# Optimization experiments

Hardware: AMD Instinct MI355X
Metric: run time of the kernel (lower is better)

The kernel has to match this reference:

```python
import jax, jax.numpy as jnp
import numpy as np

B, T, C, H = 512, 256, 512, 64  # batch, block_size, n_embedding, head_size


def setup_inputs() -> dict:
    key = jax.random.key(0)
    kx, kq, kk, kv = jax.random.split(key, 4)
    # nn.Linear(C, H, bias=False) default init ~ U(-1/sqrt(C), 1/sqrt(C)); stored as x @ W
    s = 1.0 / np.sqrt(C)
    return {
        "x": jax.random.normal(kx, (B, T, C), dtype=jnp.float32),
        "Wq": jax.random.uniform(kq, (C, H), jnp.float32, -s, s),
        "Wk": jax.random.uniform(kk, (C, H), jnp.float32, -s, s),
        "Wv": jax.random.uniform(kv, (C, H), jnp.float32, -s, s),
    }


def reference(x, Wq, Wk, Wv):
    # Projections (bias=False Linear)
    q = x @ Wq  # [B,T,H]
    k = x @ Wk  # [B,T,H]
    v = x @ Wv  # [B,T,H]
    scale = k.shape[-1] ** -0.5
    wei = jnp.einsum('bqh,bkh->bqk', q, k) * scale  # [B,T,T]
    causal = jnp.tril(jnp.ones((x.shape[1], x.shape[1]), dtype=bool))
    wei = jnp.where(causal, wei, -jnp.inf)
    wei = jax.nn.softmax(wei, axis=-1)
    # dropout p=0.0 (eval-mode reference) -> identity
    return wei @ v  # [B,T,H]
```

## Files before the change

### kernel.cpp

```cpp
#include <hip/hip_runtime.h>
#include <hip/hip_bf16.h>

typedef __bf16 bf16;
typedef __bf16 bf16x8 __attribute__((ext_vector_type(8)));
typedef __bf16 bf16x4 __attribute__((ext_vector_type(4)));
typedef float  f32x4  __attribute__((ext_vector_type(4)));

#define MFMA16(a,b,c) __builtin_amdgcn_mfma_f32_16x16x32_bf16((a),(b),(c),0,0,0)

__device__ __forceinline__ void gld16(const void* g, void* l) {
    __builtin_amdgcn_global_load_lds(
        (const __attribute__((address_space(1))) void*)g,
        (__attribute__((address_space(3))) void*)l, 16, 0, 0);
}


__global__ void __launch_bounds__(256) wt_frag_kernel(
        const float* __restrict__ Wq, const float* __restrict__ Wk,
        const float* __restrict__ Wv, bf16* __restrict__ WTfrag) {
    int tid = blockIdx.x * 256 + threadIdx.x;
    int j  = tid & 7;
    int l  = (tid >> 3) & 63;
    int f  = tid >> 9;
    int nf = f % 12;
    int KC = f / 12;
    int k   = KC * 32 + (l >> 4) * 8 + j;
    int col = (nf & 3) * 16 + (l & 15);
    const float* W = (nf < 4) ? Wq : ((nf < 8) ? Wk : Wv);
    WTfrag[tid] = (bf16)W[k * 64 + col];
}

__global__ void __launch_bounds__(256, 2) fused_kernel(
        const float* __restrict__ x, const bf16* __restrict__ WTfrag,
        float* __restrict__ out) {
    extern __shared__ char smem[];

    const int tid = threadIdx.x;
    const int l   = tid & 63;
    const int w   = tid >> 6;
    const int lo  = l & 15;
    const int hi  = l >> 4;
    const int b   = blockIdx.x;
    const char* xb = (const char*)x + (size_t)b * 524288;
    const char* wb = (const char*)WTfrag;

    f32x4 acc[4][12];
    #pragma unroll
    for (int mq = 0; mq < 4; ++mq)
        #pragma unroll
        for (int nf = 0; nf < 12; ++nf)
            acc[mq][nf] = (f32x4){0.f, 0.f, 0.f, 0.f};

    #pragma unroll 1
    for (int kc = 0; kc < 16; ++kc) {
        #pragma unroll
        for (int j = 0; j < 8; ++j) {
            const int s   = j * 256 + tid;
            const int row = s >> 3;
            const int uP  = s & 7;
            const int uL  = uP ^ (row & 7);
            gld16(xb + (size_t)row * 2048 + kc * 128 + uL * 16,
                  smem + s * 16);
        }
        #pragma unroll
        for (int j = 0; j < 3; ++j) {
            const int s = j * 256 + tid;
            gld16(wb + kc * 12288 + s * 16, smem + 32768 + s * 16);
        }
        __syncthreads();

        bf16x8 a[4];
        #pragma unroll
        for (int mq = 0; mq < 4; ++mq) {
            const int row = mq * 64 + w * 16 + lo;
            const int u0  = (hi * 2)     ^ (lo & 7);
            const int u1  = (hi * 2 + 1) ^ (lo & 7);
            f32x4 v0 = *(const f32x4*)(smem + row * 128 + u0 * 16);
            f32x4 v1 = *(const f32x4*)(smem + row * 128 + u1 * 16);
            bf16x8 t;
            t[0] = (bf16)v0[0]; t[1] = (bf16)v0[1]; t[2] = (bf16)v0[2]; t[3] = (bf16)v0[3];
            t[4] = (bf16)v1[0]; t[5] = (bf16)v1[1]; t[6] = (bf16)v1[2]; t[7] = (bf16)v1[3];
            a[mq] = t;
        }
        #pragma unroll
        for (int nf = 0; nf < 12; ++nf) {
            bf16x8 bf_ = *(const bf16x8*)(smem + 32768 + nf * 1024 + l * 16);
            #pragma unroll
            for (int mq = 0; mq < 4; ++mq)
                acc[mq][nf] = MFMA16(a[mq], bf_, acc[mq][nf]);
        }
        __syncthreads();
    }

    char* Kb = smem;
    char* Vb = smem + 32768;
    #pragma unroll
    for (int nf = 4; nf < 12; ++nf) {
        #pragma unroll
        for (int mq = 0; mq < 4; ++mq) {
            #pragma unroll
            for (int i = 0; i < 4; ++i) {
                bf16 v = (bf16)acc[mq][nf][i];
                if (nf < 8) {
                    const int row = mq * 64 + w * 16 + hi * 4 + i;
                    const int col = (nf - 4) * 16 + lo;
                    const int u   = col >> 3;
                    *(bf16*)(Kb + row * 128 + ((u ^ (row & 7)) << 4) +
                             (col & 7) * 2) = v;
                } else {
                    const int h = (nf - 8) * 16 + lo;
                    const int t = mq * 64 + w * 16 + hi * 4 + i;
                    const int u = t >> 3;
                    *(bf16*)(Vb + h * 512 + ((u ^ (h & 7)) << 4) +
                             (t & 7) * 2) = v;
                }
            }
        }
    }

    bf16* Pl = (bf16*)(smem + 65536) + w * 1152;
    bf16x8 qfr[4][2];
    #pragma unroll
    for (int qf = 0; qf < 4; ++qf) {
        #pragma unroll
        for (int nf = 0; nf < 4; ++nf)
            #pragma unroll
            for (int i = 0; i < 4; ++i)
                Pl[(hi * 4 + i) * 72 + nf * 16 + lo] = (bf16)acc[qf][nf][i];
        __syncthreads();
        #pragma unroll
        for (int ks = 0; ks < 2; ++ks)
            qfr[qf][ks] = *(const bf16x8*)(Pl + lo * 72 + ks * 32 + hi * 8);
        __syncthreads();
    }

    f32x4 o[4][4];
    #pragma unroll
    for (int qf = 0; qf < 4; ++qf)
        #pragma unroll
        for (int mf = 0; mf < 4; ++mf)
            o[qf][mf] = (f32x4){0.f, 0.f, 0.f, 0.f};
    float m2[4]   = {-INFINITY, -INFINITY, -INFINITY, -INFINITY};
    float lsum[4] = {0.f, 0.f, 0.f, 0.f};

    const float SC = 0.125f * 1.44269504088896340736f;

    #pragma unroll
    for (int kc = 0; kc < 4; ++kc) {
        bf16x8 vf[4][2];
        #pragma unroll
        for (int mf = 0; mf < 4; ++mf)
            #pragma unroll
            for (int ks = 0; ks < 2; ++ks) {
                const int h = mf * 16 + lo;
                const int u = kc * 8 + ks * 4 + hi;
                vf[mf][ks] = *(const bf16x8*)(Vb + h * 512 + ((u ^ (lo & 7)) << 4));
            }

        #pragma unroll
        for (int qf = kc; qf < 4; ++qf) {
            f32x4 s[4];
            #pragma unroll
            for (int kf = 0; kf < 4; ++kf) {
                const int key = kc * 64 + kf * 16 + lo;
                bf16x8 k0 = *(const bf16x8*)(Kb + key * 128 + ((hi ^ (lo & 7)) << 4));
                bf16x8 k1 = *(const bf16x8*)(Kb + key * 128 + (((4 + hi) ^ (lo & 7)) << 4));
                f32x4 t = (f32x4){0.f, 0.f, 0.f, 0.f};
                t = MFMA16(k0, qfr[qf][0], t);
                t = MFMA16(k1, qfr[qf][1], t);
                s[kf] = t;
            }
            float mx = -INFINITY;
            #pragma unroll
            for (int kf = 0; kf < 4; ++kf)
                #pragma unroll
                for (int i = 0; i < 4; ++i) {
                    float v = s[kf][i] * SC;
                    if (kc == qf && (kf * 16 + hi * 4 + i) > (w * 16 + lo)) v = -INFINITY;
                    s[kf][i] = v;
                    mx = fmaxf(mx, v);
                }
            mx = fmaxf(mx, __shfl_xor(mx, 16));
            mx = fmaxf(mx, __shfl_xor(mx, 32));
            const float mnew = fmaxf(m2[qf], mx);
            const float rsc  = exp2f(m2[qf] - mnew);
            m2[qf] = mnew;

            float cs = 0.f;
            bf16x4 pk[4];
            #pragma unroll
            for (int kf = 0; kf < 4; ++kf)
                #pragma unroll
                for (int i = 0; i < 4; ++i) {
                    float p = exp2f(s[kf][i] - mnew);
                    cs += p;
                    pk[kf][i] = (bf16)p;
                }
            cs += __shfl_xor(cs, 16);
            cs += __shfl_xor(cs, 32);
            lsum[qf] = lsum[qf] * rsc + cs;

            #pragma unroll
            for (int kf = 0; kf < 4; ++kf)
                *(bf16x4*)(Pl + lo * 72 + kf * 16 + hi * 4) = pk[kf];

            #pragma unroll
            for (int mf = 0; mf < 4; ++mf) {
                o[qf][mf][0] *= rsc; o[qf][mf][1] *= rsc;
                o[qf][mf][2] *= rsc; o[qf][mf][3] *= rsc;
            }
            #pragma unroll
            for (int ks = 0; ks < 2; ++ks) {
                bf16x8 pf = *(const bf16x8*)(Pl + lo * 72 + ks * 32 + hi * 8);
                #pragma unroll
                for (int mf = 0; mf < 4; ++mf)
                    o[qf][mf] = MFMA16(vf[mf][ks], pf, o[qf][mf]);
            }
        }
    }

    #pragma unroll
    for (int qf = 0; qf < 4; ++qf) {
        const float inv = 1.0f / lsum[qf];
        const int q = qf * 64 + w * 16 + lo;
        #pragma unroll
        for (int mf = 0; mf < 4; ++mf) {
            f32x4 r4;
            r4[0] = o[qf][mf][0] * inv; r4[1] = o[qf][mf][1] * inv;
            r4[2] = o[qf][mf][2] * inv; r4[3] = o[qf][mf][3] * inv;
            *(f32x4*)(out + (b * 256 + q) * 64 + mf * 16 + hi * 4) = r4;
        }
    }
}

extern "C" void kernel_launch(void* const* d_in, const int* in_sizes, int n_in,
                              void* d_out, int out_size, void* d_ws, size_t ws_size,
                              hipStream_t stream) {
    const float* x  = (const float*)d_in[0];
    const float* Wq = (const float*)d_in[1];
    const float* Wk = (const float*)d_in[2];
    const float* Wv = (const float*)d_in[3];
    float* out = (float*)d_out;

    bf16* WTfrag = (bf16*)d_ws;

    wt_frag_kernel<<<dim3(384), dim3(256), 0, stream>>>(Wq, Wk, Wv, WTfrag);
    fused_kernel<<<dim3(512), dim3(256), 74752, stream>>>(x, WTfrag, out);
}
```

Measured before the change: 71.81 us.

## Double-buffer x tiles in LDS and load weight fragments directly to registers

The projection loop now prefetches the next x chunk into a second LDS buffer while the current chunk is used for MFMA, so global load latency can overlap compute. Weight fragments are read straight from global memory into registers instead of being staged through LDS. The intent is to cut the exposed load latency and one barrier per iteration. The cost is higher register pressure (12 B fragments held live) and per-wave global reads of the weights, which are repeated across waves.

```diff
diff --git a/kernel.cpp b/kernel.cpp
--- a/kernel.cpp
+++ b/kernel.cpp
@@ -51,43 +51,47 @@
         for (int nf = 0; nf < 12; ++nf)
             acc[mq][nf] = (f32x4){0.f, 0.f, 0.f, 0.f};
 
+    #pragma unroll
+    for (int j = 0; j < 8; ++j) {
+        const int s   = j * 256 + tid;
+        const int row = s >> 3;
+        const int uL  = (s & 7) ^ (row & 7);
+        gld16(xb + (size_t)row * 2048 + 0 * 128 + uL * 16, smem + s * 16);
+    }
+    __syncthreads();
+
     #pragma unroll 1
     for (int kc = 0; kc < 16; ++kc) {
-        #pragma unroll
-        for (int j = 0; j < 8; ++j) {
-            const int s   = j * 256 + tid;
-            const int row = s >> 3;
-            const int uP  = s & 7;
-            const int uL  = uP ^ (row & 7);
-            gld16(xb + (size_t)row * 2048 + kc * 128 + uL * 16,
-                  smem + s * 16);
-        }
-        #pragma unroll
-        for (int j = 0; j < 3; ++j) {
-            const int s = j * 256 + tid;
-            gld16(wb + kc * 12288 + s * 16, smem + 32768 + s * 16);
-        }
-        __syncthreads();
-
-        bf16x8 a[4];
+        bf16x8 bfr[12];
+        #pragma unroll
+        for (int nf = 0; nf < 12; ++nf)
+            bfr[nf] = *(const bf16x8*)(wb + (kc * 12 + nf) * 1024 + l * 16);
+        __builtin_amdgcn_sched_barrier(0);
+        if (kc < 15) {
+            #pragma unroll
+            for (int j = 0; j < 8; ++j) {
+                const int s   = j * 256 + tid;
+                const int row = s >> 3;
+                const int uL  = (s & 7) ^ (row & 7);
+                gld16(xb + (size_t)row * 2048 + (kc + 1) * 128 + uL * 16,
+                      smem + ((kc + 1) & 1) * 32768 + s * 16);
+            }
+        }
+        __builtin_amdgcn_sched_barrier(0);
+        const char* xlds = smem + (kc & 1) * 32768;
         #pragma unroll
         for (int mq = 0; mq < 4; ++mq) {
             const int row = mq * 64 + w * 16 + lo;
             const int u0  = (hi * 2)     ^ (lo & 7);
             const int u1  = (hi * 2 + 1) ^ (lo & 7);
-            f32x4 v0 = *(const f32x4*)(smem + row * 128 + u0 * 16);
-            f32x4 v1 = *(const f32x4*)(smem + row * 128 + u1 * 16);
-            bf16x8 t;
-            t[0] = (bf16)v0[0]; t[1] = (bf16)v0[1]; t[2] = (bf16)v0[2]; t[3] = (bf16)v0[3];
-            t[4] = (bf16)v1[0]; t[5] = (bf16)v1[1]; t[6] = (bf16)v1[2]; t[7] = (bf16)v1[3];
-            a[mq] = t;
-        }
-        #pragma unroll
-        for (int nf = 0; nf < 12; ++nf) {
-            bf16x8 bf_ = *(const bf16x8*)(smem + 32768 + nf * 1024 + l * 16);
-            #pragma unroll
-            for (int mq = 0; mq < 4; ++mq)
-                acc[mq][nf] = MFMA16(a[mq], bf_, acc[mq][nf]);
+            f32x4 v0 = *(const f32x4*)(xlds + row * 128 + u0 * 16);
+            f32x4 v1 = *(const f32x4*)(xlds + row * 128 + u1 * 16);
+            bf16x8 a;
+            a[0] = (bf16)v0[0]; a[1] = (bf16)v0[1]; a[2] = (bf16)v0[2]; a[3] = (bf16)v0[3];
+            a[4] = (bf16)v1[0]; a[5] = (bf16)v1[1]; a[6] = (bf16)v1[2]; a[7] = (bf16)v1[3];
+            #pragma unroll
+            for (int nf = 0; nf < 12; ++nf)
+                acc[mq][nf] = MFMA16(a, bfr[nf], acc[mq][nf]);
         }
         __syncthreads();
     }
```

Result: slower. 131.9 us (+83.7%).
